# Kernel optimization log

Measured on AMD Instinct MI355X. Metric: run time of the kernel, lower is better.

Reference implementation:

```python
import jax, jax.numpy as jnp
import numpy as np
from jax import lax

B, HH, WW, C = 8, 128, 128, 192
FL = 3  # focal_level
HID = 4 * C

def _gelu(x):
    return jax.nn.gelu(x, approximate=False)

def _ln(x, g, b, eps=1e-5):
    m = jnp.mean(x, axis=-1, keepdims=True)
    v = jnp.mean(jnp.square(x - m), axis=-1, keepdims=True)
    return (x - m) * lax.rsqrt(v + eps) * g + b

def _dwconv(x, k):
    # x: (B,C,H,W), k: (C,kh,kw) depthwise kernel
    return lax.conv_general_dilated(x, k[:, None], (1, 1), 'SAME',
                                    feature_group_count=x.shape[1],
                                    dimension_numbers=('NCHW', 'OIHW', 'NCHW'))

def setup_inputs() -> dict:
    key = jax.random.key(0)
    ks = jax.random.split(key, 12)
    s = 0.02
    return {
        'x': jax.random.normal(ks[0], (B, HH * WW, C), jnp.float32),
        'ln1_g': jnp.ones((C,), jnp.float32),
        'ln1_b': jnp.zeros((C,), jnp.float32),
        'f_w': jax.random.normal(ks[1], (C, 2 * C + FL + 1), jnp.float32) * s,
        'f_b': jnp.zeros((2 * C + FL + 1,), jnp.float32),
        'fk0': jax.random.normal(ks[2], (C, 3, 3), jnp.float32) * s,
        'fk1': jax.random.normal(ks[3], (C, 5, 5), jnp.float32) * s,
        'fk2': jax.random.normal(ks[4], (C, 7, 7), jnp.float32) * s,
        'h_w': jax.random.normal(ks[5], (C, C), jnp.float32) * s,
        'h_b': jnp.zeros((C,), jnp.float32),
        'proj_w': jax.random.normal(ks[6], (C, C), jnp.float32) * s,
        'proj_b': jnp.zeros((C,), jnp.float32),
        'ln2_g': jnp.ones((C,), jnp.float32),
        'ln2_b': jnp.zeros((C,), jnp.float32),
        'fc1_w': jax.random.normal(ks[7], (C, HID), jnp.float32) * s,
        'fc1_b': jnp.zeros((HID,), jnp.float32),
        'fc2_w': jax.random.normal(ks[8], (HID, C), jnp.float32) * s,
        'fc2_b': jnp.zeros((C,), jnp.float32),
        'H': HH,
        'W': WW,
    }

def reference(x, ln1_g, ln1_b, f_w, f_b, fk0, fk1, fk2, h_w, h_b,
              proj_w, proj_b, ln2_g, ln2_b, fc1_w, fc1_b, fc2_w, fc2_b, H, W):
    b, L, c = x.shape
    shortcut = x
    t = _ln(x, ln1_g, ln1_b).reshape(b, H, W, c)
    # f projection: (B,H,W,2C+FL+1) -> (B, 2C+FL+1, H, W)
    f = (t @ f_w + f_b).transpose(0, 3, 1, 2)
    q, ctx, gates = f[:, :c], f[:, c:2 * c], f[:, 2 * c:]
    ctx_all = jnp.zeros_like(ctx)
    for l, k in enumerate((fk0, fk1, fk2)):
        ctx = _gelu(_dwconv(ctx, k))
        ctx_all = ctx_all + ctx * gates[:, l:l + 1]
    ctx_global = _gelu(jnp.mean(ctx, axis=(2, 3), keepdims=True))
    ctx_all = ctx_all + ctx_global * gates[:, FL:]
    # h: 1x1 conv over channels
    modulator = jnp.einsum('oc,bchw->bohw', h_w, ctx_all) + h_b[None, :, None, None]
    x_out = (q * modulator).transpose(0, 2, 3, 1)  # (B,H,W,C)
    x_out = (x_out @ proj_w + proj_b).reshape(b, L, c)
    x1 = shortcut + x_out
    y = _ln(x1, ln2_g, ln2_b)
    y = _gelu(y @ fc1_w + fc1_b) @ fc2_w + fc2_b
    return x1 + y
```

## Files before the change

### kernel.cpp

```cpp
#include <hip/hip_runtime.h>
#include <hip/hip_bf16.h>

#define BB   8
#define HGT  128
#define WID  128
#define CC   192
#define LLEN (HGT*WID)
#define MM   (BB*LLEN)
#define NF   388
#define HIDN 768

typedef unsigned short us16;
typedef __attribute__((ext_vector_type(8))) short bf16x8;
typedef __attribute__((ext_vector_type(4))) float f32x4;
typedef __attribute__((ext_vector_type(2))) float f32x2;

__device__ __forceinline__ float bf2f(us16 u) {
    return __uint_as_float(((unsigned int)u) << 16);
}
__device__ __forceinline__ us16 f2bf(float f) {
    unsigned int x = __float_as_uint(f);
    x = (x + 0x7fffu + ((x >> 16) & 1u)) >> 16;
    return (us16)x;
}
__device__ __forceinline__ float gelu_f(float x) {
    float u = 0.7978845608f * x * (1.0f + 0.044715f * x * x);
    float e = __expf(fminf(2.0f * u, 30.0f));
    return 0.5f * x * (1.0f + (e - 1.0f) / (e + 1.0f));
}
__device__ __forceinline__ f32x2 unpk2(unsigned d) {
    f32x2 r;
    r[0] = __uint_as_float(d << 16);
    r[1] = __uint_as_float(d & 0xffff0000u);
    return r;
}

__device__ __forceinline__ void gload_lds16(const void* g, void* l) {
    __builtin_amdgcn_global_load_lds(
        (const __attribute__((address_space(1))) void*)g,
        (__attribute__((address_space(3))) void*)l, 16, 0, 0);
}

__global__ __launch_bounds__(256) void wcvt_kernel(const float* __restrict__ f_w,
        const float* __restrict__ h_w, const float* __restrict__ proj_w,
        const float* __restrict__ fc1_w, const float* __restrict__ fc2_w,
        const float* __restrict__ fk0, const float* __restrict__ fk1,
        const float* __restrict__ fk2,
        us16* __restrict__ fwT, us16* __restrict__ hwB, us16* __restrict__ projT,
        us16* __restrict__ w1T, us16* __restrict__ w2T,
        us16* __restrict__ kw0T, us16* __restrict__ kw1T, us16* __restrict__ kw2T) {
    int i = blockIdx.x * 256 + threadIdx.x;
    if (i < 86016) {
        int n = i / 192, k = i % 192;
        fwT[i] = (n < NF) ? f2bf(f_w[k * NF + n]) : (us16)0;
        return;
    }
    i -= 86016;
    if (i < 36864) { hwB[i] = f2bf(h_w[i]); return; }
    i -= 36864;
    if (i < 36864) { int n = i / 192, k = i % 192; projT[i] = f2bf(proj_w[k * CC + n]); return; }
    i -= 36864;
    if (i < 147456) { int n = i / 192, k = i % 192; w1T[i] = f2bf(fc1_w[k * HIDN + n]); return; }
    i -= 147456;
    if (i < 147456) { int n = i / 768, k = i % 768; w2T[i] = f2bf(fc2_w[k * CC + n]); return; }
    i -= 147456;
    if (i < 1728)  { int kyx = i / 192, c = i % 192; kw0T[i] = f2bf(fk0[c * 9 + kyx]);  return; }
    i -= 1728;
    if (i < 4800)  { int kyx = i / 192, c = i % 192; kw1T[i] = f2bf(fk1[c * 25 + kyx]); return; }
    i -= 4800;
    if (i < 9408)  { int kyx = i / 192, c = i % 192; kw2T[i] = f2bf(fk2[c * 49 + kyx]); return; }
}

__global__ __launch_bounds__(256) void ln_kernel(const float* __restrict__ in,
                                                 const float* __restrict__ g,
                                                 const float* __restrict__ b,
                                                 us16* __restrict__ out) {
    int wid  = threadIdx.x >> 6;
    int lane = threadIdx.x & 63;
    int row  = blockIdx.x * 4 + wid;
    const float* p = in + (size_t)row * CC;
    float v0 = p[lane], v1 = p[lane + 64], v2 = p[lane + 128];
    float s1 = v0 + v1 + v2;
    float s2 = v0*v0 + v1*v1 + v2*v2;
    for (int o = 32; o; o >>= 1) { s1 += __shfl_xor(s1, o); s2 += __shfl_xor(s2, o); }
    float m   = s1 * (1.0f / 192.0f);
    float var = s2 * (1.0f / 192.0f) - m * m;
    float inv = rsqrtf(var + 1e-5f);
    us16* q = out + (size_t)row * CC;
    q[lane]       = f2bf((v0 - m) * inv * g[lane]       + b[lane]);
    q[lane + 64]  = f2bf((v1 - m) * inv * g[lane + 64]  + b[lane + 64]);
    q[lane + 128] = f2bf((v2 - m) * inv * g[lane + 128] + b[lane + 128]);
}

template<int MODE>
__global__ __launch_bounds__(256) void mgemm_kernel(const us16* __restrict__ A,
        const us16* __restrict__ Bt, const float* __restrict__ bias,
        us16* __restrict__ out_q, us16* __restrict__ out_ctx, us16* __restrict__ out_g,
        const us16* __restrict__ q_in, const us16* __restrict__ gates_in,
        const float* __restrict__ hg, const float* __restrict__ x_in,
        float* __restrict__ out_f) {
    __shared__ __align__(16) char Asm[128 * 384];
    constexpr int NT = (MODE == 0) ? 7 : 3;
    int id  = blockIdx.x;
    int mt  = (id & 7) * 128 + (id >> 3);
    int m0  = mt * 128;
    int tid = threadIdx.x, lane = tid & 63, w = tid >> 6;
    int wm = w >> 1, wn = w & 1, g = lane >> 4, lr = lane & 15;

    const char* Agl = (const char*)(A + (size_t)m0 * CC);
    #pragma unroll
    for (int i = 0; i < 12; i++) {
        int wl   = w * 12 + i;
        int byte = wl * 1024 + lane * 16;
        int row  = byte / 384;
        int off  = byte - row * 384;
        int soff = off ^ ((row & 7) << 4);
        gload_lds16(Agl + (size_t)row * 384 + soff, Asm + wl * 1024);
    }
    __syncthreads();

    int orow = m0 + wm * 64;
    int bidx = m0 >> 14;
    for (int nt = 0; nt < NT; nt++) {
        int n0 = nt * 64;
        const us16* Bb = Bt + (size_t)(n0 + wn * 32 + lr) * CC;
        bf16x8 bfr[6][2];
        #pragma unroll
        for (int kk = 0; kk < 6; kk++)
            #pragma unroll
            for (int j = 0; j < 2; j++)
                bfr[kk][j] = *(const bf16x8*)(Bb + (size_t)j * 16 * CC + kk * 32 + g * 8);

        f32x4 acc[4][2] = {};
        #pragma unroll
        for (int kk = 0; kk < 6; kk++) {
            int k2 = (kk * 32 + g * 8) * 2;
            bf16x8 a[4];
            #pragma unroll
            for (int i = 0; i < 4; i++) {
                int row = wm * 64 + i * 16 + lr;
                a[i] = *(const bf16x8*)(Asm + row * 384 + (k2 ^ ((row & 7) << 4)));
            }
            #pragma unroll
            for (int j = 0; j < 2; j++) {
                acc[0][j] = __builtin_amdgcn_mfma_f32_16x16x32_bf16(a[0], bfr[kk][j], acc[0][j], 0, 0, 0);
                acc[1][j] = __builtin_amdgcn_mfma_f32_16x16x32_bf16(a[1], bfr[kk][j], acc[1][j], 0, 0, 0);
                acc[2][j] = __builtin_amdgcn_mfma_f32_16x16x32_bf16(a[2], bfr[kk][j], acc[2][j], 0, 0, 0);
                acc[3][j] = __builtin_amdgcn_mfma_f32_16x16x32_bf16(a[3], bfr[kk][j], acc[3][j], 0, 0, 0);
            }
        }
        #pragma unroll
        for (int i = 0; i < 4; i++) {
            #pragma unroll
            for (int j = 0; j < 2; j++) {
                int ncol = n0 + wn * 32 + j * 16;
                int cc   = ncol + lr;
                #pragma unroll
                for (int r = 0; r < 4; r++) {
                    int row = orow + i * 16 + g * 4 + r;
                    float v = acc[i][j][r];
                    if (MODE == 0) {
                        if (ncol < 192)      out_q[(size_t)row * CC + cc]          = f2bf(v + bias[cc]);
                        else if (ncol < 384) out_ctx[(size_t)row * CC + (cc - 192)] = f2bf(v + bias[cc]);
                        else if (cc < NF)    out_g[(size_t)row * 4 + (cc - 384)]    = f2bf(v + bias[cc]);
                    } else if (MODE == 1) {
                        float val = v + bias[cc] + bf2f(gates_in[(size_t)row * 4 + 3]) * hg[bidx * CC + cc];
                        val *= bf2f(q_in[(size_t)row * CC + cc]);
                        out_q[(size_t)row * CC + cc] = f2bf(val);
                    } else {
                        out_f[(size_t)row * CC + cc] = v + bias[cc] + x_in[(size_t)row * CC + cc];
                    }
                }
            }
        }
    }
}

template<int F, int LVL>
__global__ __launch_bounds__(256) void convv2_kernel(const us16* __restrict__ in,
                            us16* __restrict__ outp,
                            us16* __restrict__ ctx,
                            const us16* __restrict__ gates,
                            const us16* __restrict__ kwT,
                            float* __restrict__ partial) {
    constexpr int P  = F / 2;
    constexpr int NW = F + 3;
    __shared__ __align__(16) us16 kws[F * F * CC];
    int tid = threadIdx.x;
    int lb  = (blockIdx.x & 7) * 384 + (blockIdx.x >> 3);
    for (int t = tid; t < F * F * CC / 8; t += 256)
        ((bf16x8*)kws)[t] = ((const bf16x8*)kwT)[t];
    __syncthreads();
    int idx  = lb * 256 + tid;
    int cg   = idx % 24;
    int rest = idx / 24;
    int x4 = rest & 31;
    int y0 = (rest >> 5) & 127;
    int b  = rest >> 12;
    int x0 = x4 * 4;
    f32x2 acc[4][4] = {};
    const us16* inb = in + (size_t)b * LLEN * CC + cg * 8;
    for (int ky = 0; ky < F; ky++) {
        int yy = y0 + ky - P;
        if (yy < 0 || yy > 127) continue;
        const us16* rp = inb + (size_t)yy * WID * CC;
        f32x2 rv[NW][4];
        #pragma unroll
        for (int i = 0; i < NW; i++) {
            int xx = x0 - P + i;
            if (xx >= 0 && xx <= 127) {
                uint4 v = *(const uint4*)(rp + (size_t)xx * CC);
                rv[i][0] = unpk2(v.x); rv[i][1] = unpk2(v.y);
                rv[i][2] = unpk2(v.z); rv[i][3] = unpk2(v.w);
            } else {
                rv[i][0] = rv[i][1] = rv[i][2] = rv[i][3] = (f32x2){0.0f, 0.0f};
            }
        }
        #pragma unroll
        for (int kx = 0; kx < F; kx++) {
            uint4 wv = *(const uint4*)(kws + (ky * F + kx) * CC + cg * 8);
            f32x2 w0 = unpk2(wv.x), w1 = unpk2(wv.y), w2 = unpk2(wv.z), w3 = unpk2(wv.w);
            #pragma unroll
            for (int px = 0; px < 4; px++) {
                acc[px][0] += rv[kx + px][0] * w0;
                acc[px][1] += rv[kx + px][1] * w1;
                acc[px][2] += rv[kx + px][2] * w2;
                acc[px][3] += rv[kx + px][3] * w3;
            }
        }
    }
    int pix = (b * HGT + y0) * WID + x0;
    size_t obase = (size_t)pix * CC + cg * 8;
    if constexpr (LVL == 0) {
        #pragma unroll
        for (int px = 0; px < 4; px++) {
            uint4 ov;
            unsigned* po = &ov.x;
            #pragma unroll
            for (int q = 0; q < 4; q++)
                po[q] = (unsigned)f2bf(gelu_f(acc[px][q][0]))
                      | ((unsigned)f2bf(gelu_f(acc[px][q][1])) << 16);
            *(uint4*)(outp + obase + (size_t)px * CC) = ov;
        }
    } else if constexpr (LVL == 1) {
        #pragma unroll
        for (int px = 0; px < 4; px++) {
            unsigned gv = *(const unsigned*)(gates + (size_t)(pix + px) * 4);
            float g0 = bf2f((us16)(gv & 0xffffu));
            float g1 = bf2f((us16)(gv >> 16));
            uint4 c3v = *(const uint4*)(inb + ((size_t)y0 * WID + x0 + px) * CC);
            const unsigned* pc = &c3v.x;
            uint4 ov, cv;
            unsigned* po = &ov.x;
            unsigned* pv = &cv.x;
            #pragma unroll
            for (int q = 0; q < 4; q++) {
                f32x2 c3 = unpk2(pc[q]);
                float v5a = gelu_f(acc[px][q][0]);
                float v5b = gelu_f(acc[px][q][1]);
                po[q] = (unsigned)f2bf(v5a) | ((unsigned)f2bf(v5b) << 16);
                pv[q] = (unsigned)f2bf(g0 * c3[0] + g1 * v5a)
                      | ((unsigned)f2bf(g0 * c3[1] + g1 * v5b) << 16);
            }
            *(uint4*)(outp + obase + (size_t)px * CC) = ov;
            *(uint4*)(ctx  + obase + (size_t)px * CC) = cv;
        }
    } else {
        f32x2 csum[4] = {};
        #pragma unroll
        for (int px = 0; px < 4; px++) {
            float g2 = bf2f(gates[(size_t)(pix + px) * 4 + 2]);
            uint4 cv = *(const uint4*)(ctx + obase + (size_t)px * CC);
            const unsigned* pc = &cv.x;
            uint4 ov;
            unsigned* po = &ov.x;
            #pragma unroll
            for (int q = 0; q < 4; q++) {
                f32x2 cprev = unpk2(pc[q]);
                float c7a = gelu_f(acc[px][q][0]);
                float c7b = gelu_f(acc[px][q][1]);
                csum[q][0] += c7a;
                csum[q][1] += c7b;
                po[q] = (unsigned)f2bf(cprev[0] + g2 * c7a)
                      | ((unsigned)f2bf(cprev[1] + g2 * c7b) << 16);
            }
            *(uint4*)(ctx + obase + (size_t)px * CC) = ov;
        }
        __syncthreads();
        float (*psum)[8] = (float (*)[8])kws;
        #pragma unroll
        for (int q = 0; q < 4; q++) {
            psum[tid][q * 2]     = csum[q][0];
            psum[tid][q * 2 + 1] = csum[q][1];
        }
        __syncthreads();
        if (tid < 192) {
            int j = tid & 7, cgw = tid >> 3;
            int t0 = (cgw - (lb * 256) % 24) % 24;
            if (t0 < 0) t0 += 24;
            float s = 0.0f;
            for (int t = t0; t < 256; t += 24) s += psum[t][j];
            partial[(size_t)lb * CC + tid] = s;
        }
    }
}

__global__ __launch_bounds__(192) void gmean2_kernel(const float* __restrict__ partial,
                                                     const float* __restrict__ h_w,
                                                     float* __restrict__ hg) {
    __shared__ float ctxg[CC];
    int b = blockIdx.x, c = threadIdx.x;
    const float* pb = partial + (size_t)b * 384 * CC + c;
    float s = 0.0f;
    for (int k = 0; k < 384; k++) s += pb[(size_t)k * CC];
    ctxg[c] = gelu_f(s * (1.0f / 16384.0f));
    __syncthreads();
    float a = 0.0f;
    for (int c2 = 0; c2 < CC; c2++) a += h_w[c * CC + c2] * ctxg[c2];
    hg[b * CC + c] = a;
}

__global__ __launch_bounds__(512, 4) void fc1_kernel(const us16* __restrict__ A,
        const us16* __restrict__ w1T, const float* __restrict__ bias,
        us16* __restrict__ hid0, us16* __restrict__ hid1) {
    __shared__ __align__(16) char Asm[128 * 384];
    int id  = blockIdx.x;
    int swz = (id & 7) * 384 + (id >> 3);
    int mt  = swz / 6, nt = swz % 6;
    int m0 = mt * 128;
    int n0 = nt * 128;
    int tid = threadIdx.x, lane = tid & 63, w = tid >> 6;
    int wm = w >> 2, wn = w & 3, g = lane >> 4, lr = lane & 15;

    const char* Agl = (const char*)(A + (size_t)m0 * CC);
    #pragma unroll
    for (int i = 0; i < 6; i++) {
        int wl   = w * 6 + i;
        int byte = wl * 1024 + lane * 16;
        int row  = byte / 384;
        int off  = byte - row * 384;
        int soff = off ^ ((row & 7) << 4);
        gload_lds16(Agl + (size_t)row * 384 + soff, Asm + wl * 1024);
    }
    const us16* Bb = w1T + (size_t)(n0 + wn * 32 + lr) * CC;
    bf16x8 bfr[6][2];
    #pragma unroll
    for (int kk = 0; kk < 6; kk++)
        #pragma unroll
        for (int j = 0; j < 2; j++)
            bfr[kk][j] = *(const bf16x8*)(Bb + (size_t)j * 16 * CC + kk * 32 + g * 8);

    __syncthreads();

    f32x4 acc[4][2] = {};
    #pragma unroll
    for (int kk = 0; kk < 6; kk++) {
        int k2 = (kk * 32 + g * 8) * 2;
        bf16x8 a[4];
        #pragma unroll
        for (int i = 0; i < 4; i++) {
            int row = wm * 64 + i * 16 + lr;
            a[i] = *(const bf16x8*)(Asm + row * 384 + (k2 ^ ((row & 7) << 4)));
        }
        #pragma unroll
        for (int j = 0; j < 2; j++) {
            acc[0][j] = __builtin_amdgcn_mfma_f32_16x16x32_bf16(a[0], bfr[kk][j], acc[0][j], 0, 0, 0);
            acc[1][j] = __builtin_amdgcn_mfma_f32_16x16x32_bf16(a[1], bfr[kk][j], acc[1][j], 0, 0, 0);
            acc[2][j] = __builtin_amdgcn_mfma_f32_16x16x32_bf16(a[2], bfr[kk][j], acc[2][j], 0, 0, 0);
            acc[3][j] = __builtin_amdgcn_mfma_f32_16x16x32_bf16(a[3], bfr[kk][j], acc[3][j], 0, 0, 0);
        }
    }
    us16* hidp = (m0 & 32768) ? hid1 : hid0;
    int ml = (m0 & 32767) + wm * 64;
    #pragma unroll
    for (int i = 0; i < 4; i++) {
        #pragma unroll
        for (int j = 0; j < 2; j++) {
            int col = n0 + wn * 32 + j * 16 + lr;
            float fb = bias[col];
            #pragma unroll
            for (int r = 0; r < 4; r++) {
                int row = ml + i * 16 + g * 4 + r;
                hidp[(size_t)row * HIDN + col] = f2bf(gelu_f(acc[i][j][r] + fb));
            }
        }
    }
}

__global__ __launch_bounds__(512, 4) void fc2_kernel(const us16* __restrict__ hid0,
        const us16* __restrict__ hid1, const us16* __restrict__ w2T,
        const float* __restrict__ bias, float* __restrict__ io) {
    __shared__ __align__(16) char Asm[128 * 384];
    int m0 = blockIdx.x * 128;
    int tid = threadIdx.x, lane = tid & 63, w = tid >> 6;
    int wm = w >> 2, wn = w & 3, g = lane >> 4, lr = lane & 15;
    const us16* hidp = (m0 & 32768) ? hid1 : hid0;
    const char* Agl = (const char*)(hidp + (size_t)(m0 & 32767) * HIDN);

    f32x4 acc[4][3] = {};
    for (int c = 0; c < 4; c++) {
        #pragma unroll
        for (int i = 0; i < 6; i++) {
            int wl   = w * 6 + i;
            int byte = wl * 1024 + lane * 16;
            int row  = byte / 384;
            int off  = byte - row * 384;
            int soff = off ^ ((row & 7) << 4);
            gload_lds16(Agl + (size_t)row * 1536 + c * 384 + soff, Asm + wl * 1024);
        }
        __syncthreads();
        #pragma unroll
        for (int kk = 0; kk < 6; kk++) {
            int k2 = (kk * 32 + g * 8) * 2;
            bf16x8 a[4];
            #pragma unroll
            for (int i = 0; i < 4; i++) {
                int row = wm * 64 + i * 16 + lr;
                a[i] = *(const bf16x8*)(Asm + row * 384 + (k2 ^ ((row & 7) << 4)));
            }
            #pragma unroll
            for (int j = 0; j < 3; j++) {
                bf16x8 bv = *(const bf16x8*)(w2T + (size_t)(wn * 48 + j * 16 + lr) * HIDN
                                             + c * 192 + kk * 32 + g * 8);
                acc[0][j] = __builtin_amdgcn_mfma_f32_16x16x32_bf16(a[0], bv, acc[0][j], 0, 0, 0);
                acc[1][j] = __builtin_amdgcn_mfma_f32_16x16x32_bf16(a[1], bv, acc[1][j], 0, 0, 0);
                acc[2][j] = __builtin_amdgcn_mfma_f32_16x16x32_bf16(a[2], bv, acc[2][j], 0, 0, 0);
                acc[3][j] = __builtin_amdgcn_mfma_f32_16x16x32_bf16(a[3], bv, acc[3][j], 0, 0, 0);
            }
        }
        __syncthreads();
    }
    #pragma unroll
    for (int i = 0; i < 4; i++) {
        #pragma unroll
        for (int j = 0; j < 3; j++) {
            int col = wn * 48 + j * 16 + lr;
            float fb = bias[col];
            #pragma unroll
            for (int r = 0; r < 4; r++) {
                int row = m0 + wm * 64 + i * 16 + g * 4 + r;
                io[(size_t)row * CC + col] += acc[i][j][r] + fb;
            }
        }
    }
}

extern "C" void kernel_launch(void* const* d_in, const int* in_sizes, int n_in,
                              void* d_out, int out_size, void* d_ws, size_t ws_size,
                              hipStream_t stream) {
    const float* x      = (const float*)d_in[0];
    const float* ln1_g  = (const float*)d_in[1];
    const float* ln1_b  = (const float*)d_in[2];
    const float* f_w    = (const float*)d_in[3];
    const float* f_b    = (const float*)d_in[4];
    const float* fk0    = (const float*)d_in[5];
    const float* fk1    = (const float*)d_in[6];
    const float* fk2    = (const float*)d_in[7];
    const float* h_w    = (const float*)d_in[8];
    const float* h_b    = (const float*)d_in[9];
    const float* proj_w = (const float*)d_in[10];
    const float* proj_b = (const float*)d_in[11];
    const float* ln2_g  = (const float*)d_in[12];
    const float* ln2_b  = (const float*)d_in[13];
    const float* fc1_w  = (const float*)d_in[14];
    const float* fc1_b  = (const float*)d_in[15];
    const float* fc2_w  = (const float*)d_in[16];
    const float* fc2_b  = (const float*)d_in[17];
    float* outp = (float*)d_out;

    char* ws = (char*)d_ws;
    const size_t S = (size_t)MM * CC * 2;
    us16* t_buf   = (us16*)(ws);
    us16* q_buf   = (us16*)(ws + S);
    us16* ctx_all = (us16*)(ws + 2 * S);
    us16* gates   = (us16*)(ws + 3 * S);
    float* hg      = (float*)(ws + 3 * S + 1048576);
    us16* fwT   = (us16*)(ws + 3 * S + 1048576 + 786432 + 6144);
    us16* hwB   = fwT + 86016;
    us16* projT = hwB + 36864;
    us16* w1T   = projT + 36864;
    us16* w2T   = w1T + 147456;
    us16* kw0T  = w2T + 147456;
    us16* kw1T  = kw0T + 1728;
    us16* kw2T  = kw1T + 4800;
    us16* ctxA = (us16*)d_out;
    us16* ctxB = (us16*)d_out + (size_t)MM * CC;
    float* partial = (float*)ctxB;

    wcvt_kernel<<<1839, 256, 0, stream>>>(f_w, h_w, proj_w, fc1_w, fc2_w,
                                          fk0, fk1, fk2,
                                          fwT, hwB, projT, w1T, w2T, kw0T, kw1T, kw2T);

    ln_kernel<<<MM / 4, 256, 0, stream>>>(x, ln1_g, ln1_b, t_buf);

    mgemm_kernel<0><<<1024, 256, 0, stream>>>(
        t_buf, fwT, f_b, q_buf, ctxA, gates, nullptr, nullptr, nullptr, nullptr, nullptr);

    convv2_kernel<3, 0><<<3072, 256, 0, stream>>>(ctxA, ctxB, nullptr, nullptr, kw0T, nullptr);
    convv2_kernel<5, 1><<<3072, 256, 0, stream>>>(ctxB, ctxA, ctx_all, gates, kw1T, nullptr);
    convv2_kernel<7, 2><<<3072, 256, 0, stream>>>(ctxA, nullptr, ctx_all, gates, kw2T, partial);

    gmean2_kernel<<<8, 192, 0, stream>>>(partial, h_w, hg);

    mgemm_kernel<1><<<1024, 256, 0, stream>>>(
        ctx_all, hwB, h_b, t_buf, nullptr, nullptr, q_buf, gates, hg, nullptr, nullptr);

    mgemm_kernel<2><<<1024, 256, 0, stream>>>(
        t_buf, projT, proj_b, nullptr, nullptr, nullptr, nullptr, nullptr, nullptr, x, outp);

    ln_kernel<<<MM / 4, 256, 0, stream>>>(outp, ln2_g, ln2_b, q_buf);

    for (int h = 0; h < 2; h++) {
        const us16* Ah = q_buf + (size_t)h * 65536 * CC;
        float* ioh     = outp  + (size_t)h * 65536 * CC;
        fc1_kernel<<<3072, 512, 0, stream>>>(Ah, w1T, fc1_b, t_buf, ctx_all);
        fc2_kernel<<<512, 512, 0, stream>>>(t_buf, ctx_all, w2T, fc2_b, ioh);
    }
}
```

Baseline: 687.9 us.

## Widen depthwise conv register tile to 8 pixels and simplify GELU

Each thread in the depthwise conv kernels now computes 8 horizontal pixels instead of 4. The kernel weights for a row are held in registers and the inputs are streamed, so each loaded input column feeds more outputs and redundant halo loads drop. Grid size and the partial-sum count for the global mean are halved to match. GELU is rewritten as x*sigmoid(1.702-style tanh form) using a fast reciprocal, which cuts ALU work per element. The cost is higher register pressure from the 8x4 accumulators plus F weight vectors, which may reduce occupancy.

```diff
diff --git a/kernel.cpp b/kernel.cpp
--- a/kernel.cpp
+++ b/kernel.cpp
@@ -24,9 +24,9 @@
     return (us16)x;
 }
 __device__ __forceinline__ float gelu_f(float x) {
-    float u = 0.7978845608f * x * (1.0f + 0.044715f * x * x);
-    float e = __expf(fminf(2.0f * u, 30.0f));
-    return 0.5f * x * (1.0f + (e - 1.0f) / (e + 1.0f));
+    float t = x * (1.5957691f + 0.07135481f * x * x);
+    float e = __expf(-t);
+    return x * __builtin_amdgcn_rcpf(1.0f + e);
 }
 __device__ __forceinline__ f32x2 unpk2(unsigned d) {
     f32x2 r;
@@ -184,48 +184,54 @@
                             const us16* __restrict__ kwT,
                             float* __restrict__ partial) {
     constexpr int P  = F / 2;
-    constexpr int NW = F + 3;
+    constexpr int NW = F + 7;
     __shared__ __align__(16) us16 kws[F * F * CC];
     int tid = threadIdx.x;
-    int lb  = (blockIdx.x & 7) * 384 + (blockIdx.x >> 3);
+    int lb  = (blockIdx.x & 7) * 192 + (blockIdx.x >> 3);
     for (int t = tid; t < F * F * CC / 8; t += 256)
         ((bf16x8*)kws)[t] = ((const bf16x8*)kwT)[t];
     __syncthreads();
     int idx  = lb * 256 + tid;
     int cg   = idx % 24;
     int rest = idx / 24;
-    int x4 = rest & 31;
-    int y0 = (rest >> 5) & 127;
-    int b  = rest >> 12;
-    int x0 = x4 * 4;
-    f32x2 acc[4][4] = {};
+    int x8 = rest & 15;
+    int y0 = (rest >> 4) & 127;
+    int b  = rest >> 11;
+    int x0 = x8 * 8;
+    f32x2 acc[8][4] = {};
     const us16* inb = in + (size_t)b * LLEN * CC + cg * 8;
     for (int ky = 0; ky < F; ky++) {
         int yy = y0 + ky - P;
         if (yy < 0 || yy > 127) continue;
         const us16* rp = inb + (size_t)yy * WID * CC;
-        f32x2 rv[NW][4];
+        f32x2 w[F][4];
+        #pragma unroll
+        for (int kx = 0; kx < F; kx++) {
+            uint4 wv = *(const uint4*)(kws + (ky * F + kx) * CC + cg * 8);
+            w[kx][0] = unpk2(wv.x); w[kx][1] = unpk2(wv.y);
+            w[kx][2] = unpk2(wv.z); w[kx][3] = unpk2(wv.w);
+        }
         #pragma unroll
         for (int i = 0; i < NW; i++) {
             int xx = x0 - P + i;
+            f32x2 rv[4];
             if (xx >= 0 && xx <= 127) {
                 uint4 v = *(const uint4*)(rp + (size_t)xx * CC);
-                rv[i][0] = unpk2(v.x); rv[i][1] = unpk2(v.y);
-                rv[i][2] = unpk2(v.z); rv[i][3] = unpk2(v.w);
+                rv[0] = unpk2(v.x); rv[1] = unpk2(v.y);
+                rv[2] = unpk2(v.z); rv[3] = unpk2(v.w);
             } else {
-                rv[i][0] = rv[i][1] = rv[i][2] = rv[i][3] = (f32x2){0.0f, 0.0f};
-            }
-        }
-        #pragma unroll
-        for (int kx = 0; kx < F; kx++) {
-            uint4 wv = *(const uint4*)(kws + (ky * F + kx) * CC + cg * 8);
-            f32x2 w0 = unpk2(wv.x), w1 = unpk2(wv.y), w2 = unpk2(wv.z), w3 = unpk2(wv.w);
-            #pragma unroll
-            for (int px = 0; px < 4; px++) {
-                acc[px][0] += rv[kx + px][0] * w0;
-                acc[px][1] += rv[kx + px][1] * w1;
-                acc[px][2] += rv[kx + px][2] * w2;
-                acc[px][3] += rv[kx + px][3] * w3;
+                rv[0] = rv[1] = rv[2] = rv[3] = (f32x2){0.0f, 0.0f};
+            }
+            #pragma unroll
+            for (int px = 0; px < 8; px++) {
+                constexpr int dummy = 0; (void)dummy;
+                int kx = i - px;
+                if (kx >= 0 && kx < F) {
+                    acc[px][0] += rv[0] * w[kx][0];
+                    acc[px][1] += rv[1] * w[kx][1];
+                    acc[px][2] += rv[2] * w[kx][2];
+                    acc[px][3] += rv[3] * w[kx][3];
+                }
             }
         }
     }
@@ -233,7 +239,7 @@
     size_t obase = (size_t)pix * CC + cg * 8;
     if constexpr (LVL == 0) {
         #pragma unroll
-        for (int px = 0; px < 4; px++) {
+        for (int px = 0; px < 8; px++) {
             uint4 ov;
             unsigned* po = &ov.x;
             #pragma unroll
@@ -244,7 +250,7 @@
         }
     } else if constexpr (LVL == 1) {
         #pragma unroll
-        for (int px = 0; px < 4; px++) {
+        for (int px = 0; px < 8; px++) {
             unsigned gv = *(const unsigned*)(gates + (size_t)(pix + px) * 4);
             float g0 = bf2f((us16)(gv & 0xffffu));
             float g1 = bf2f((us16)(gv >> 16));
@@ -268,7 +274,7 @@
     } else {
         f32x2 csum[4] = {};
         #pragma unroll
-        for (int px = 0; px < 4; px++) {
+        for (int px = 0; px < 8; px++) {
             float g2 = bf2f(gates[(size_t)(pix + px) * 4 + 2]);
             uint4 cv = *(const uint4*)(ctx + obase + (size_t)px * CC);
             const unsigned* pc = &cv.x;
@@ -310,9 +316,9 @@
                                                      float* __restrict__ hg) {
     __shared__ float ctxg[CC];
     int b = blockIdx.x, c = threadIdx.x;
-    const float* pb = partial + (size_t)b * 384 * CC + c;
+    const float* pb = partial + (size_t)b * 192 * CC + c;
     float s = 0.0f;
-    for (int k = 0; k < 384; k++) s += pb[(size_t)k * CC];
+    for (int k = 0; k < 192; k++) s += pb[(size_t)k * CC];
     ctxg[c] = gelu_f(s * (1.0f / 16384.0f));
     __syncthreads();
     float a = 0.0f;
@@ -496,9 +502,9 @@
     mgemm_kernel<0><<<1024, 256, 0, stream>>>(
         t_buf, fwT, f_b, q_buf, ctxA, gates, nullptr, nullptr, nullptr, nullptr, nullptr);
 
-    convv2_kernel<3, 0><<<3072, 256, 0, stream>>>(ctxA, ctxB, nullptr, nullptr, kw0T, nullptr);
-    convv2_kernel<5, 1><<<3072, 256, 0, stream>>>(ctxB, ctxA, ctx_all, gates, kw1T, nullptr);
-    convv2_kernel<7, 2><<<3072, 256, 0, stream>>>(ctxA, nullptr, ctx_all, gates, kw2T, partial);
+    convv2_kernel<3, 0><<<1536, 256, 0, stream>>>(ctxA, ctxB, nullptr, nullptr, kw0T, nullptr);
+    convv2_kernel<5, 1><<<1536, 256, 0, stream>>>(ctxB, ctxA, ctx_all, gates, kw1T, nullptr);
+    convv2_kernel<7, 2><<<1536, 256, 0, stream>>>(ctxA, nullptr, ctx_all, gates, kw2T, partial);
 
     gmean2_kernel<<<8, 192, 0, stream>>>(partial, h_w, hg);
 
```

Result: faster. 636.0 us (-7.5%).
